# Kernel optimization log

Measured on AMD Instinct MI355X. Metric: run time of the kernel, lower is better.

## Reference

```python
import jax, jax.numpy as jnp
import numpy as np

N, E, D, H = 100000, 1000000, 64, 4
HD = D // H  # head dim
G = 64       # num graphs in batch
EPS = 1e-5
NEG_SLOPE = 0.2


def setup_inputs() -> dict:
    key = jax.random.key(0)
    ks = jax.random.split(key, 10)
    x = jax.random.normal(ks[0], (N, D), dtype=jnp.float32)
    edge_index = jax.random.randint(ks[1], (2, E), 0, N)
    batch = jnp.sort(jax.random.randint(ks[2], (N,), 0, G))
    s = 1.0 / np.sqrt(D)
    Wl = jax.random.uniform(ks[3], (D, D), jnp.float32, -s, s)   # lin_l (source)
    Wr = jax.random.uniform(ks[4], (D, D), jnp.float32, -s, s)   # lin_r (target)
    att = jax.random.uniform(ks[5], (H, HD), jnp.float32, -s, s)
    bias_gat = jnp.zeros((D,), jnp.float32)
    gn_weight = jnp.ones((D,), jnp.float32)
    gn_bias = jnp.zeros((D,), jnp.float32)
    gn_mean_scale = jnp.ones((D,), jnp.float32)
    return {"x": x, "edge_index": edge_index, "batch": batch, "Wl": Wl,
            "Wr": Wr, "att": att, "bias_gat": bias_gat, "gn_weight": gn_weight,
            "gn_bias": gn_bias, "gn_mean_scale": gn_mean_scale}


def _gatv2(x, src, dst, Wl, Wr, att, bias_gat):
    # per-node linear projections, reshaped to heads
    xl = (x @ Wl).reshape(N, H, HD)  # source features
    xr = (x @ Wr).reshape(N, H, HD)  # target features
    # per-edge attention logits: a^T LeakyReLU(xl_j + xr_i)
    e = xl[src] + xr[dst]                             # [E', H, HD]
    e = jnp.where(e >= 0, e, NEG_SLOPE * e)           # leaky_relu
    score = jnp.einsum('ehd,hd->eh', e, att)          # [E', H]
    # segment softmax over incoming edges of each dst node
    m = jax.ops.segment_max(score, dst, num_segments=N)   # [N, H]
    p = jnp.exp(score - m[dst])
    denom = jax.ops.segment_sum(p, dst, num_segments=N)   # [N, H]
    alpha = p / denom[dst]                                # [E', H]
    # weighted scatter-add aggregation of source features
    out = jax.ops.segment_sum(alpha[:, :, None] * xl[src], dst, num_segments=N)
    return out.reshape(N, D) + bias_gat


def _graph_norm(h, batch, weight, bias, mean_scale):
    cnt = jax.ops.segment_sum(jnp.ones((N,), h.dtype), batch, num_segments=G)
    cnt = jnp.maximum(cnt, 1.0)[:, None]                      # [G,1]
    mean = jax.ops.segment_sum(h, batch, num_segments=G) / cnt
    out = h - mean_scale * mean[batch]
    var = jax.ops.segment_sum(out * out, batch, num_segments=G) / cnt
    return weight * out / jnp.sqrt(var[batch] + EPS) + bias


def reference(x, edge_index, batch, Wl, Wr, att, bias_gat, gn_weight, gn_bias, gn_mean_scale):
    # eval mode: dropout / DropEdge are identity; pre_norm=False; res_proj=Identity
    loops = jnp.arange(N)
    src = jnp.concatenate([edge_index[0], loops])  # add self-loops (PyG default)
    dst = jnp.concatenate([edge_index[1], loops])
    h = _gatv2(x, src, dst, Wl, Wr, att, bias_gat)
    h = h + x                                       # identity residual
    h = jnp.where(h > 0, h, jnp.expm1(h))           # ELU
    h = _graph_norm(h, batch, gn_weight, gn_bias, gn_mean_scale)
    return h
```

## Files before the change

### kernel.cpp

```cpp
#include <hip/hip_runtime.h>
#include <hip/hip_bf16.h>
#include <math.h>

#define G_ 64
#define NEG_SLOPE 0.2f
#define EPS_ 1e-5f
#define BBITS 7
#define BSZ 128
#define CAP 2048
#define EPB 2048

typedef __attribute__((ext_vector_type(8))) unsigned short ushort8;
typedef __attribute__((ext_vector_type(8))) short bf16x8;
typedef __attribute__((ext_vector_type(4))) float f32x4;

#define DPP_ADD(t, ctrl)                                                   \
  do {                                                                     \
    int _p = __builtin_amdgcn_update_dpp(0, __float_as_int(t), (ctrl),     \
                                         0xf, 0xf, true);                  \
    (t) += __int_as_float(_p);                                             \
  } while (0)
#define REDUCE8(t)                                                         \
  do {                                                                     \
    DPP_ADD(t, 0xB1);                                                      \
    DPP_ADD(t, 0x4E);                                                      \
    DPP_ADD(t, 0x141);                                                     \
  } while (0)

__device__ __forceinline__ float leaky_(float e) {
  return 0.6f * e + 0.4f * fabsf(e);
}

__device__ __forceinline__ short f2bf(float f) {
  __hip_bfloat16 h = __float2bfloat16(f);
  return *reinterpret_cast<short*>(&h);
}

__global__ __launch_bounds__(64) void prepack_kernel(
    const float* __restrict__ Wl, const float* __restrict__ Wr,
    bf16x8* __restrict__ bpack) {
  const int lane = threadIdx.x;
  const int lrow = lane & 15;
  const int lgrp = lane >> 4;
#pragma unroll
  for (int ct = 0; ct < 8; ++ct) {
    const float* W = (ct < 4) ? Wl : Wr;
    const int col = ((ct & 3) * 16) + lrow;
#pragma unroll
    for (int kk = 0; kk < 2; ++kk) {
      const int kb = kk * 32 + lgrp * 8;
      bf16x8 f;
#pragma unroll
      for (int j = 0; j < 8; ++j) f[j] = f2bf(W[(kb + j) * 64 + col]);
      bpack[(ct * 2 + kk) * 64 + lane] = f;
    }
  }
}

__global__ __launch_bounds__(256) void proj_mfma_kernel(
    const float* __restrict__ x, const bf16x8* __restrict__ bpack,
    __hip_bfloat16* __restrict__ xlb, __hip_bfloat16* __restrict__ xrb,
    int n) {
  const int lane = threadIdx.x & 63;
  const int wv = threadIdx.x >> 6;
  const int rbase = blockIdx.x * 64 + wv * 16;
  const int lrow = lane & 15;
  const int lgrp = lane >> 4;

  bf16x8 bfrag[8][2];
#pragma unroll
  for (int ct = 0; ct < 8; ++ct)
#pragma unroll
    for (int kk = 0; kk < 2; ++kk)
      bfrag[ct][kk] = bpack[(ct * 2 + kk) * 64 + lane];

  bf16x8 afrag[2];
  const int r = rbase + lrow;
#pragma unroll
  for (int kk = 0; kk < 2; ++kk) {
    bf16x8 f;
    if (r < n) {
      const float4* p = (const float4*)(x + (size_t)r * 64 + kk * 32 + lgrp * 8);
      float4 u = p[0], v = p[1];
      f[0] = f2bf(u.x); f[1] = f2bf(u.y); f[2] = f2bf(u.z); f[3] = f2bf(u.w);
      f[4] = f2bf(v.x); f[5] = f2bf(v.y); f[6] = f2bf(v.z); f[7] = f2bf(v.w);
    } else {
      f = bf16x8{0, 0, 0, 0, 0, 0, 0, 0};
    }
    afrag[kk] = f;
  }

  f32x4 acc[8];
#pragma unroll
  for (int ct = 0; ct < 8; ++ct) acc[ct] = f32x4{0.f, 0.f, 0.f, 0.f};
#pragma unroll
  for (int ct = 0; ct < 8; ++ct)
#pragma unroll
    for (int kk = 0; kk < 2; ++kk)
      acc[ct] = __builtin_amdgcn_mfma_f32_16x16x32_bf16(
          afrag[kk], bfrag[ct][kk], acc[ct], 0, 0, 0);

#pragma unroll
  for (int ct = 0; ct < 8; ++ct) {
    __hip_bfloat16* dst = (ct < 4) ? xlb : xrb;
    const int c = ((ct & 3) * 16) + lrow;
#pragma unroll
    for (int j = 0; j < 4; ++j) {
      const int rr = rbase + lgrp * 4 + j;
      if (rr < n) dst[(size_t)rr * 64 + c] = __float2bfloat16(acc[ct][j]);
    }
  }
}

__global__ __launch_bounds__(256) void bucket_kernel(
    const int* __restrict__ esrc, const int* __restrict__ edst,
    int* __restrict__ bcnt, unsigned int* __restrict__ packed,
    int e, int nb) {
  __shared__ int cnt[800];
  __shared__ int base[800];
  const int t = threadIdx.x;
  const int e0 = blockIdx.x * EPB;
  const int e1 = (e0 + EPB) < e ? (e0 + EPB) : e;
  for (int b = t; b < nb; b += 256) cnt[b] = 0;
  __syncthreads();
  for (int i = e0 + t; i < e1; i += 256)
    atomicAdd(&cnt[edst[i] >> BBITS], 1);
  __syncthreads();
  for (int b = t; b < nb; b += 256) {
    int c = cnt[b];
    base[b] = c ? atomicAdd(&bcnt[b], c) : 0;
    cnt[b] = 0;
  }
  __syncthreads();
  for (int i = e0 + t; i < e1; i += 256) {
    int d = edst[i];
    int b = d >> BBITS;
    int pos = base[b] + atomicAdd(&cnt[b], 1);
    if (pos < CAP)
      packed[(size_t)b * CAP + pos] =
          ((unsigned)(d & (BSZ - 1)) << 17) | (unsigned)esrc[i];
  }
}

__global__ __launch_bounds__(256) void sort_kernel(
    unsigned int* __restrict__ packed, const int* __restrict__ bcnt,
    int2* __restrict__ nse, int n) {
  __shared__ unsigned int stage[CAP];
  __shared__ int cnt[BSZ];
  __shared__ int sc[BSZ];
  __shared__ int off[BSZ + 1];
  const int t = threadIdx.x;
  const int b = blockIdx.x;
  int ecnt = bcnt[b];
  if (ecnt > CAP) ecnt = CAP;
  for (int j = t; j < ecnt; j += 256) stage[j] = packed[(size_t)b * CAP + j];
  if (t < BSZ) cnt[t] = 0;
  __syncthreads();
  for (int j = t; j < ecnt; j += 256) atomicAdd(&cnt[stage[j] >> 17], 1);
  __syncthreads();
  if (t < BSZ) sc[t] = cnt[t];
  __syncthreads();
#pragma unroll
  for (int o = 1; o < BSZ; o <<= 1) {
    int v = 0;
    if (t < BSZ && t >= o) v = sc[t - o];
    __syncthreads();
    if (t < BSZ) sc[t] += v;
    __syncthreads();
  }
  if (t < BSZ) {
    off[t + 1] = sc[t];
    if (t == 0) off[0] = 0;
    cnt[t] = sc[t] - cnt[t];
  }
  __syncthreads();
  for (int j = t; j < ecnt; j += 256) {
    unsigned v = stage[j];
    int pos = atomicAdd(&cnt[v >> 17], 1);
    packed[(size_t)b * CAP + pos] = v & 0x1FFFF;
  }
  const int nodebase = b << BBITS;
  if (t < BSZ && nodebase + t < n) {
    int s = off[t];
    nse[nodebase + t] = make_int2(b * CAP + s, off[t + 1] - s);
  }
}

template <int NB>
__device__ __forceinline__ void burst_(
    const char* xbase, unsigned poff, int myedge, int half, int tot,
    float xr0, float xr1, float a0, float a1,
    float& acc0, float& acc1, float& den) {
  unsigned vv[NB];
#pragma unroll
  for (int j = 0; j < NB; ++j) {
    const int sa = __builtin_amdgcn_readlane(myedge, 2 * j);
    const int sb = __builtin_amdgcn_readlane(myedge, 2 * j + 1);
    const int s = half ? sb : sa;
    vv[j] = *(const unsigned*)(xbase + (((unsigned)s << 7) | poff));
  }
#pragma unroll
  for (int j = 0; j < NB; ++j) {
    const unsigned v = vv[j];
    const float l0 = __uint_as_float(v << 16);
    const float l1 = __uint_as_float(v & 0xFFFF0000u);
    float e0 = leaky_(l0 + xr0);
    float e1 = leaky_(l1 + xr1);
    float t = a0 * e0 + a1 * e1;
    REDUCE8(t);
    float p = exp2f(t);
    p = ((2 * j + half) < tot) ? p : 0.f;
    acc0 = fmaf(p, l0, acc0);
    acc1 = fmaf(p, l1, acc1);
    den += p;
  }
}

__global__ __launch_bounds__(256) void aggregate_kernel(
    const __hip_bfloat16* __restrict__ xlb,
    const __hip_bfloat16* __restrict__ xrb, const float* __restrict__ x,
    const float* __restrict__ att, const float* __restrict__ bias_gat,
    const int2* __restrict__ nse, const unsigned int* __restrict__ srt,
    __hip_bfloat16* __restrict__ hb, int n) {
  const int lane = threadIdx.x & 63;
  const int i = (blockIdx.x * blockDim.x + threadIdx.x) >> 6;
  if (i >= n) return;
  const int pos = lane & 31;
  const int half = lane >> 5;
  const float2 attp = ((const float2*)att)[pos];
  const float a0 = attp.x * 1.44269504f;
  const float a1 = attp.y * 1.44269504f;
  const unsigned xr_pk = ((const unsigned*)(xrb + (size_t)i * 64))[pos];
  const float xr0 = __uint_as_float(xr_pk << 16);
  const float xr1 = __uint_as_float(xr_pk & 0xFFFF0000u);
  int2 sd = nse[i];
  const int s0 = __builtin_amdgcn_readfirstlane(sd.x);
  const int deg = __builtin_amdgcn_readfirstlane(sd.y);
  const int tot = deg + 1;
  int myedge = i;
  if (lane > 0 && lane < tot) myedge = (int)srt[s0 + lane - 1];
  float acc0 = 0.f, acc1 = 0.f, den = 0.f;
  const char* xbase = (const char*)xlb;
  const unsigned poff = (unsigned)pos << 2;

  if (tot <= 8) {
    burst_<4>(xbase, poff, myedge, half, tot, xr0, xr1, a0, a1,
              acc0, acc1, den);
  } else {
    burst_<8>(xbase, poff, myedge, half, tot, xr0, xr1, a0, a1,
              acc0, acc1, den);
    const int kmax = tot < 64 ? tot : 64;
    for (int k = 16; k < kmax; k += 2) {
      const int sa = __builtin_amdgcn_readlane(myedge, k);
      const int sb = (k + 1 < kmax) ? __builtin_amdgcn_readlane(myedge, k + 1)
                                    : sa;
      const int s = half ? sb : sa;
      const unsigned v = *(const unsigned*)(xbase + (((unsigned)s << 7) | poff));
      const float l0 = __uint_as_float(v << 16);
      const float l1 = __uint_as_float(v & 0xFFFF0000u);
      float e0 = leaky_(l0 + xr0);
      float e1 = leaky_(l1 + xr1);
      float t = a0 * e0 + a1 * e1;
      REDUCE8(t);
      float p = exp2f(t);
      p = ((k + half) < kmax) ? p : 0.f;
      acc0 = fmaf(p, l0, acc0);
      acc1 = fmaf(p, l1, acc1);
      den += p;
    }
    for (int kk = 64; kk < tot; ++kk) {
      const int s = (int)srt[s0 + kk - 1];
      const unsigned v = *(const unsigned*)(xbase + (((unsigned)s << 7) | poff));
      const float l0 = __uint_as_float(v << 16);
      const float l1 = __uint_as_float(v & 0xFFFF0000u);
      float e0 = leaky_(l0 + xr0);
      float e1 = leaky_(l1 + xr1);
      float t = a0 * e0 + a1 * e1;
      REDUCE8(t);
      float p = exp2f(t);
      p = half ? 0.f : p;
      acc0 = fmaf(p, l0, acc0);
      acc1 = fmaf(p, l1, acc1);
      den += p;
    }
  }

  acc0 += __shfl_xor(acc0, 32);
  acc1 += __shfl_xor(acc1, 32);
  den += __shfl_xor(den, 32);
  if (half == 0) {
    const float inv = 1.f / den;
    const float2 xres = ((const float2*)(x + (size_t)i * 64))[pos];
    const float2 bb = ((const float2*)bias_gat)[pos];
    float h0 = fmaf(acc0, inv, bb.x) + xres.x;
    float h1 = fmaf(acc1, inv, bb.y) + xres.y;
    h0 = h0 > 0.f ? h0 : expm1f(h0);
    h1 = h1 > 0.f ? h1 : expm1f(h1);
    __hip_bfloat16 b0 = __float2bfloat16(h0);
    __hip_bfloat16 b1 = __float2bfloat16(h1);
    unsigned pk = ((unsigned)(*(unsigned short*)&b1) << 16) |
                  (unsigned)(*(unsigned short*)&b0);
    ((unsigned*)(hb + (size_t)i * 64))[pos] = pk;
  }
}

__global__ __launch_bounds__(256) void gsum2_kernel(
    const __hip_bfloat16* __restrict__ h, const int* __restrict__ batch,
    float* __restrict__ gsum, float* __restrict__ gsq,
    float* __restrict__ gcnt, int n) {
  const int lane = threadIdx.x & 63;
  const int wave = (blockIdx.x * blockDim.x + threadIdx.x) >> 6;
  const int nwaves = (gridDim.x * blockDim.x) >> 6;
  const int chunk = (n + nwaves - 1) / nwaves;
  const int start = wave * chunk;
  const int end = (start + chunk) < n ? (start + chunk) : n;
  float s1 = 0.f, s2 = 0.f, cntl = 0.f;
  int curg = -1;
  for (int i = start; i < end; ++i) {
    int g = batch[i];
    if (g != curg) {
      if (curg >= 0) {
        atomicAdd(&gsum[curg * 64 + lane], s1);
        atomicAdd(&gsq[curg * 64 + lane], s2);
        if (lane == 0) atomicAdd(&gcnt[curg], cntl);
      }
      curg = g; s1 = 0.f; s2 = 0.f; cntl = 0.f;
    }
    float hv = __bfloat162float(h[(size_t)i * 64 + lane]);
    s1 += hv;
    s2 += hv * hv;
    cntl += 1.f;
  }
  if (curg >= 0) {
    atomicAdd(&gsum[curg * 64 + lane], s1);
    atomicAdd(&gsq[curg * 64 + lane], s2);
    if (lane == 0) atomicAdd(&gcnt[curg], cntl);
  }
}

__global__ void stats_kernel(const float* __restrict__ gsum,
                             const float* __restrict__ gsq,
                             const float* __restrict__ gcnt,
                             const float* __restrict__ mscale,
                             const float* __restrict__ w,
                             float* __restrict__ msmean,
                             float* __restrict__ scale) {
  int i = blockIdx.x * blockDim.x + threadIdx.x;
  if (i < G_ * 64) {
    int dd = i & 63;
    float c = gcnt[i >> 6];
    c = c > 1.f ? c : 1.f;
    float mean = gsum[i] / c;
    float ms = mscale[dd];
    float var = gsq[i] / c - ms * (2.f - ms) * mean * mean;
    msmean[i] = ms * mean;
    scale[i] = w[dd] * rsqrtf(var + EPS_);
  }
}

__global__ __launch_bounds__(256) void out_kernel(
    const __hip_bfloat16* __restrict__ hb, const int* __restrict__ batch,
    const float* __restrict__ msmean, const float* __restrict__ scale,
    const float* __restrict__ bias, float* __restrict__ out, int n) {
  const int total8 = n * 8;
  for (int idx = blockIdx.x * blockDim.x + threadIdx.x; idx < total8;
       idx += gridDim.x * blockDim.x) {
    int i = idx >> 3, q = idx & 7;
    int g = batch[i];
    int base = g * 64 + q * 8;
    ushort8 hv8 = ((const ushort8*)hb)[idx];
    float r[8];
#pragma unroll
    for (int j = 0; j < 8; ++j) {
      float f = __uint_as_float(((unsigned)hv8[j]) << 16);
      r[j] = (f - msmean[base + j]) * scale[base + j] + bias[q * 8 + j];
    }
    float4 o0 = make_float4(r[0], r[1], r[2], r[3]);
    float4 o1 = make_float4(r[4], r[5], r[6], r[7]);
    ((float4*)out)[idx * 2] = o0;
    ((float4*)out)[idx * 2 + 1] = o1;
  }
}

extern "C" void kernel_launch(void* const* d_in, const int* in_sizes, int n_in,
                              void* d_out, int out_size, void* d_ws, size_t ws_size,
                              hipStream_t stream) {
  const float* x        = (const float*)d_in[0];
  const int*   eidx     = (const int*)d_in[1];
  const int*   batch    = (const int*)d_in[2];
  const float* Wl       = (const float*)d_in[3];
  const float* Wr       = (const float*)d_in[4];
  const float* att      = (const float*)d_in[5];
  const float* bias_gat = (const float*)d_in[6];
  const float* gw       = (const float*)d_in[7];
  const float* gb       = (const float*)d_in[8];
  const float* gms      = (const float*)d_in[9];
  const int N = in_sizes[0] / 64;
  const int E = in_sizes[1] / 2;
  const int* esrc = eidx;
  const int* edst = eidx + E;
  float* out = (float*)d_out;
  const int NB_ = (N + BSZ - 1) >> BBITS;

  char* wsp = (char*)d_ws;
  float* gsum   = (float*)wsp;                wsp += G_ * 64 * 4;
  float* gsq    = (float*)wsp;                wsp += G_ * 64 * 4;
  float* gcnt   = (float*)wsp;                wsp += G_ * 4;
  float* msmean = (float*)wsp;                wsp += G_ * 64 * 4;
  float* scale  = (float*)wsp;                wsp += G_ * 64 * 4;
  bf16x8* bpack = (bf16x8*)wsp;               wsp += 16 * 64 * 16;
  int*   bcnt   = (int*)wsp;                  wsp += (size_t)NB_ * 4;
  int2*  nse    = (int2*)wsp;                 wsp += (size_t)N * 8;
  unsigned int* packed = (unsigned int*)wsp;  wsp += (size_t)NB_ * CAP * 4;
  __hip_bfloat16* xlb = (__hip_bfloat16*)wsp; wsp += (size_t)N * 64 * 2;
  __hip_bfloat16* xrb = (__hip_bfloat16*)wsp; wsp += (size_t)N * 64 * 2;
  __hip_bfloat16* hb  = (__hip_bfloat16*)wsp; wsp += (size_t)N * 64 * 2;

  hipMemsetAsync(gsum, 0, (size_t)(2 * G_ * 64 + G_) * sizeof(float), stream);
  hipMemsetAsync(bcnt, 0, (size_t)NB_ * sizeof(int), stream);

  prepack_kernel<<<1, 64, 0, stream>>>(Wl, Wr, bpack);
  proj_mfma_kernel<<<(N + 63) / 64, 256, 0, stream>>>(x, bpack, xlb, xrb, N);

  const int ab = (E + EPB - 1) / EPB;
  bucket_kernel<<<ab, 256, 0, stream>>>(esrc, edst, bcnt, packed, E, NB_);
  sort_kernel<<<NB_, 256, 0, stream>>>(packed, bcnt, nse, N);

  aggregate_kernel<<<(N + 3) / 4, 256, 0, stream>>>(
      xlb, xrb, x, att, bias_gat, nse, packed, hb, N);

  gsum2_kernel<<<1024, 256, 0, stream>>>(hb, batch, gsum, gsq, gcnt, N);
  stats_kernel<<<(G_ * 64 + 255) / 256, 256, 0, stream>>>(gsum, gsq, gcnt, gms,
                                                          gw, msmean, scale);
  out_kernel<<<3125, 256, 0, stream>>>(hb, batch, msmean, scale, gb, out, N);
}
```

Measured before the change: 165.5 us.

## Merge memsets into init kernel, fold stats into output, widen stats loads

The two memsets are folded into the weight-prepack kernel, which becomes a multi-block init kernel, and the stats kernel is removed by recomputing mean and scale inside the output kernel. The intent is to cut launch and per-kernel overhead. Bucket_kernel now preloads its 8 edges per thread into registers so it reads edge indices once instead of twice. Gsum2 processes two rows per wave with packed bf16 pair loads. In exchange, out_kernel does redundant per-element rsqrt and divide work and reads more statistics arrays.

```diff
diff --git a/kernel.cpp b/kernel.cpp
--- a/kernel.cpp
+++ b/kernel.cpp
@@ -36,24 +36,34 @@
   return *reinterpret_cast<short*>(&h);
 }
 
-__global__ __launch_bounds__(64) void prepack_kernel(
+__global__ __launch_bounds__(256) void init_kernel(
     const float* __restrict__ Wl, const float* __restrict__ Wr,
-    bf16x8* __restrict__ bpack) {
-  const int lane = threadIdx.x;
-  const int lrow = lane & 15;
-  const int lgrp = lane >> 4;
-#pragma unroll
-  for (int ct = 0; ct < 8; ++ct) {
-    const float* W = (ct < 4) ? Wl : Wr;
-    const int col = ((ct & 3) * 16) + lrow;
-#pragma unroll
-    for (int kk = 0; kk < 2; ++kk) {
-      const int kb = kk * 32 + lgrp * 8;
-      bf16x8 f;
-#pragma unroll
-      for (int j = 0; j < 8; ++j) f[j] = f2bf(W[(kb + j) * 64 + col]);
-      bpack[(ct * 2 + kk) * 64 + lane] = f;
-    }
+    bf16x8* __restrict__ bpack, int* __restrict__ bcnt,
+    float* __restrict__ gzero, int nb) {
+  if (blockIdx.x == 0) {
+    const int lane = threadIdx.x;
+    if (lane < 64) {
+      const int lrow = lane & 15;
+      const int lgrp = lane >> 4;
+#pragma unroll
+      for (int ct = 0; ct < 8; ++ct) {
+        const float* W = (ct < 4) ? Wl : Wr;
+        const int col = ((ct & 3) * 16) + lrow;
+#pragma unroll
+        for (int kk = 0; kk < 2; ++kk) {
+          const int kb = kk * 32 + lgrp * 8;
+          bf16x8 f;
+#pragma unroll
+          for (int j = 0; j < 8; ++j) f[j] = f2bf(W[(kb + j) * 64 + col]);
+          bpack[(ct * 2 + kk) * 64 + lane] = f;
+        }
+      }
+    }
+  } else {
+    const int idx = (blockIdx.x - 1) * 256 + threadIdx.x;
+    const int stride = (gridDim.x - 1) * 256;
+    for (int j = idx; j < nb; j += stride) bcnt[j] = 0;
+    for (int j = idx; j < 2 * G_ * 64 + G_; j += stride) gzero[j] = 0.f;
   }
 }
 
@@ -121,10 +131,19 @@
   const int t = threadIdx.x;
   const int e0 = blockIdx.x * EPB;
   const int e1 = (e0 + EPB) < e ? (e0 + EPB) : e;
+  int dloc[8], sloc[8];
+#pragma unroll
+  for (int it = 0; it < 8; ++it) {
+    const int i = e0 + t + it * 256;
+    const bool ok = i < e1;
+    dloc[it] = ok ? edst[i] : -1;
+    sloc[it] = ok ? esrc[i] : 0;
+  }
   for (int b = t; b < nb; b += 256) cnt[b] = 0;
   __syncthreads();
-  for (int i = e0 + t; i < e1; i += 256)
-    atomicAdd(&cnt[edst[i] >> BBITS], 1);
+#pragma unroll
+  for (int it = 0; it < 8; ++it)
+    if (dloc[it] >= 0) atomicAdd(&cnt[dloc[it] >> BBITS], 1);
   __syncthreads();
   for (int b = t; b < nb; b += 256) {
     int c = cnt[b];
@@ -132,13 +151,16 @@
     cnt[b] = 0;
   }
   __syncthreads();
-  for (int i = e0 + t; i < e1; i += 256) {
-    int d = edst[i];
-    int b = d >> BBITS;
-    int pos = base[b] + atomicAdd(&cnt[b], 1);
-    if (pos < CAP)
-      packed[(size_t)b * CAP + pos] =
-          ((unsigned)(d & (BSZ - 1)) << 17) | (unsigned)esrc[i];
+#pragma unroll
+  for (int it = 0; it < 8; ++it) {
+    if (dloc[it] >= 0) {
+      const int d = dloc[it];
+      const int b = d >> BBITS;
+      const int pos = base[b] + atomicAdd(&cnt[b], 1);
+      if (pos < CAP)
+        packed[(size_t)b * CAP + pos] =
+            ((unsigned)(d & (BSZ - 1)) << 17) | (unsigned)sloc[it];
+    }
   }
 }
 
@@ -309,71 +331,75 @@
     float* __restrict__ gsum, float* __restrict__ gsq,
     float* __restrict__ gcnt, int n) {
   const int lane = threadIdx.x & 63;
+  const int pos = lane & 31;
+  const int half = lane >> 5;
   const int wave = (blockIdx.x * blockDim.x + threadIdx.x) >> 6;
   const int nwaves = (gridDim.x * blockDim.x) >> 6;
-  const int chunk = (n + nwaves - 1) / nwaves;
+  int chunk = (n + nwaves - 1) / nwaves;
+  chunk = (chunk + 1) & ~1;
   const int start = wave * chunk;
-  const int end = (start + chunk) < n ? (start + chunk) : n;
-  float s1 = 0.f, s2 = 0.f, cntl = 0.f;
+  if (start >= n) return;
+  int end = start + chunk;
+  if (end > n) end = n;
+  float s10 = 0.f, s11 = 0.f, s20 = 0.f, s21 = 0.f, cntl = 0.f;
   int curg = -1;
-  for (int i = start; i < end; ++i) {
-    int g = batch[i];
-    if (g != curg) {
-      if (curg >= 0) {
-        atomicAdd(&gsum[curg * 64 + lane], s1);
-        atomicAdd(&gsq[curg * 64 + lane], s2);
-        if (lane == 0) atomicAdd(&gcnt[curg], cntl);
+  for (int i = start; i < end; i += 2) {
+    const int row = i + half;
+    if (row < end) {
+      const int g = batch[row];
+      if (g != curg) {
+        if (curg >= 0) {
+          atomicAdd(&gsum[curg * 64 + 2 * pos], s10);
+          atomicAdd(&gsum[curg * 64 + 2 * pos + 1], s11);
+          atomicAdd(&gsq[curg * 64 + 2 * pos], s20);
+          atomicAdd(&gsq[curg * 64 + 2 * pos + 1], s21);
+          if (pos == 0) atomicAdd(&gcnt[curg], cntl);
+        }
+        curg = g;
+        s10 = 0.f; s11 = 0.f; s20 = 0.f; s21 = 0.f; cntl = 0.f;
       }
-      curg = g; s1 = 0.f; s2 = 0.f; cntl = 0.f;
-    }
-    float hv = __bfloat162float(h[(size_t)i * 64 + lane]);
-    s1 += hv;
-    s2 += hv * hv;
-    cntl += 1.f;
+      const unsigned v = ((const unsigned*)(h + (size_t)row * 64))[pos];
+      const float f0 = __uint_as_float(v << 16);
+      const float f1 = __uint_as_float(v & 0xFFFF0000u);
+      s10 += f0; s11 += f1;
+      s20 += f0 * f0; s21 += f1 * f1;
+      cntl += 1.f;
+    }
   }
   if (curg >= 0) {
-    atomicAdd(&gsum[curg * 64 + lane], s1);
-    atomicAdd(&gsq[curg * 64 + lane], s2);
-    if (lane == 0) atomicAdd(&gcnt[curg], cntl);
-  }
-}
-
-__global__ void stats_kernel(const float* __restrict__ gsum,
-                             const float* __restrict__ gsq,
-                             const float* __restrict__ gcnt,
-                             const float* __restrict__ mscale,
-                             const float* __restrict__ w,
-                             float* __restrict__ msmean,
-                             float* __restrict__ scale) {
-  int i = blockIdx.x * blockDim.x + threadIdx.x;
-  if (i < G_ * 64) {
-    int dd = i & 63;
-    float c = gcnt[i >> 6];
-    c = c > 1.f ? c : 1.f;
-    float mean = gsum[i] / c;
-    float ms = mscale[dd];
-    float var = gsq[i] / c - ms * (2.f - ms) * mean * mean;
-    msmean[i] = ms * mean;
-    scale[i] = w[dd] * rsqrtf(var + EPS_);
+    atomicAdd(&gsum[curg * 64 + 2 * pos], s10);
+    atomicAdd(&gsum[curg * 64 + 2 * pos + 1], s11);
+    atomicAdd(&gsq[curg * 64 + 2 * pos], s20);
+    atomicAdd(&gsq[curg * 64 + 2 * pos + 1], s21);
+    if (pos == 0) atomicAdd(&gcnt[curg], cntl);
   }
 }
 
 __global__ __launch_bounds__(256) void out_kernel(
     const __hip_bfloat16* __restrict__ hb, const int* __restrict__ batch,
-    const float* __restrict__ msmean, const float* __restrict__ scale,
-    const float* __restrict__ bias, float* __restrict__ out, int n) {
+    const float* __restrict__ gsum, const float* __restrict__ gsq,
+    const float* __restrict__ gcnt, const float* __restrict__ mscale,
+    const float* __restrict__ w, const float* __restrict__ bias,
+    float* __restrict__ out, int n) {
   const int total8 = n * 8;
   for (int idx = blockIdx.x * blockDim.x + threadIdx.x; idx < total8;
        idx += gridDim.x * blockDim.x) {
     int i = idx >> 3, q = idx & 7;
     int g = batch[i];
+    float c = gcnt[g];
+    c = c > 1.f ? c : 1.f;
+    float inv = 1.f / c;
     int base = g * 64 + q * 8;
     ushort8 hv8 = ((const ushort8*)hb)[idx];
     float r[8];
 #pragma unroll
     for (int j = 0; j < 8; ++j) {
+      int dd = q * 8 + j;
+      float mean = gsum[base + j] * inv;
+      float ms = mscale[dd];
+      float var = gsq[base + j] * inv - ms * (2.f - ms) * mean * mean;
       float f = __uint_as_float(((unsigned)hv8[j]) << 16);
-      r[j] = (f - msmean[base + j]) * scale[base + j] + bias[q * 8 + j];
+      r[j] = (f - ms * mean) * (w[dd] * rsqrtf(var + EPS_)) + bias[dd];
     }
     float4 o0 = make_float4(r[0], r[1], r[2], r[3]);
     float4 o1 = make_float4(r[4], r[5], r[6], r[7]);
@@ -406,8 +432,6 @@
   float* gsum   = (float*)wsp;                wsp += G_ * 64 * 4;
   float* gsq    = (float*)wsp;                wsp += G_ * 64 * 4;
   float* gcnt   = (float*)wsp;                wsp += G_ * 4;
-  float* msmean = (float*)wsp;                wsp += G_ * 64 * 4;
-  float* scale  = (float*)wsp;                wsp += G_ * 64 * 4;
   bf16x8* bpack = (bf16x8*)wsp;               wsp += 16 * 64 * 16;
   int*   bcnt   = (int*)wsp;                  wsp += (size_t)NB_ * 4;
   int2*  nse    = (int2*)wsp;                 wsp += (size_t)N * 8;
@@ -416,10 +440,7 @@
   __hip_bfloat16* xrb = (__hip_bfloat16*)wsp; wsp += (size_t)N * 64 * 2;
   __hip_bfloat16* hb  = (__hip_bfloat16*)wsp; wsp += (size_t)N * 64 * 2;
 
-  hipMemsetAsync(gsum, 0, (size_t)(2 * G_ * 64 + G_) * sizeof(float), stream);
-  hipMemsetAsync(bcnt, 0, (size_t)NB_ * sizeof(int), stream);
-
-  prepack_kernel<<<1, 64, 0, stream>>>(Wl, Wr, bpack);
+  init_kernel<<<9, 256, 0, stream>>>(Wl, Wr, bpack, bcnt, gsum, NB_);
   proj_mfma_kernel<<<(N + 63) / 64, 256, 0, stream>>>(x, bpack, xlb, xrb, N);
 
   const int ab = (E + EPB - 1) / EPB;
@@ -430,7 +451,6 @@
       xlb, xrb, x, att, bias_gat, nse, packed, hb, N);
 
   gsum2_kernel<<<1024, 256, 0, stream>>>(hb, batch, gsum, gsq, gcnt, N);
-  stats_kernel<<<(G_ * 64 + 255) / 256, 256, 0, stream>>>(gsum, gsq, gcnt, gms,
-                                                          gw, msmean, scale);
-  out_kernel<<<3125, 256, 0, stream>>>(hb, batch, msmean, scale, gb, out, N);
-}
+  out_kernel<<<3125, 256, 0, stream>>>(hb, batch, gsum, gsq, gcnt, gms, gw,
+                                       gb, out, N);
+}
```

Result: slower. 181.5 us (+9.7%).
